# Performance work log

Hardware: AMD Instinct MI355X
Metric: run time of the kernel (lower is better)

## Reference

```python
import jax, jax.numpy as jnp
import numpy as np

G, K1, K2, N, NP, EPS = 16, 128, 32, 128, 512, 1e-5

def _bn(x, axes):
    m = jnp.mean(x, axes, keepdims=True)
    v = jnp.var(x, axes, keepdims=True)  # biased, as torch BN training mode
    return (x - m) * jax.lax.rsqrt(v + EPS)

def _fps(xyz, npoint):
    # farthest point sampling, deterministic start at index 0; xyz (B,P,3)
    B, P, _ = xyz.shape
    def step(carry, _):
        dists, far = carry
        c = jnp.take_along_axis(xyz, far[:, None, None], axis=1)   # (B,1,3)
        d = jnp.sum((xyz - c) ** 2, -1)                            # (B,P)
        dists = jnp.minimum(dists, d)
        return (dists, jnp.argmax(dists, -1)), far
    init = (jnp.full((B, P), 1e10, xyz.dtype), jnp.zeros((B,), jnp.int32))
    _, idx = jax.lax.scan(step, init, None, length=npoint)         # (npoint,B)
    return jnp.take_along_axis(xyz, idx.T[:, :, None], axis=1)     # (B,npoint,3)

def _pointnet(x, w1, b1, w2, b2, w3, b3):
    h = jax.nn.relu(_bn(x @ w1 + b1, (0, 1)))
    h = jax.nn.relu(_bn(h @ w2 + b2, (0, 1)))
    h = _bn(h @ w3 + b3, (0, 1))
    return jnp.max(h, axis=1)                                      # (B,1024)

def _mapping(feat, w1, b1, w2, b2, w3, b3, w4, b4):
    # all 16 branches stacked on leading axis g
    h = jax.nn.relu(_bn(jnp.einsum('bk,gkj->gbj', feat, w1) + b1[:, None, :], (1,)))
    h = jax.nn.relu(_bn(jnp.einsum('gbj,gjk->gbk', h, w2) + b2[:, None, :], (1,)))
    h = jax.nn.relu(_bn(jnp.einsum('gbj,gjk->gbk', h, w3) + b3[:, None, :], (1,)))
    return jax.nn.relu(_bn(jnp.einsum('gbj,gjk->gbk', h, w4) + b4[:, None, :], (1,)))

def _axform(feat, fw, fb, c1w, c1b, c2w, c2b, c3w, c3b, c4w, c4b):
    # feat (G,B,K1); 1x1 convs expressed as einsums in channels-last layout
    xb = (jnp.einsum('gbk,gkm->gbm', feat, fw) + fb[:, None, :]).reshape(G, -1, N, K2)
    h = jax.nn.relu(_bn(jnp.einsum('gbnk,gkc->gbnc', xb, c1w) + c1b[:, None, None, :], (1, 2)))
    h = jax.nn.relu(_bn(jnp.einsum('gbnc,gcd->gbnd', h, c2w) + c2b[:, None, None, :], (1, 2)))
    h = jnp.einsum('gbnd,gde->gbne', h, c3w) + c3b[:, None, None, :]  # (G,B,N,1024)
    w = jax.nn.softmax(h, axis=2)                                     # softmax over N
    y = jnp.einsum('gbne,gbnk->gbek', w, xb)                          # (G,B,1024,K2)
    return jnp.einsum('gbek,gkc->gbec', y, c4w) + c4b[:, None, None, :]  # (G,B,1024,3)

def _forward(x, pn, mp, gen, ref):
    x_partial = _fps(x, NP)                                           # (B,512,3)
    feat = _pointnet(x, *pn)                                          # (B,1024)
    mfeat = _mapping(feat, *mp)                                       # (G,B,K1)
    x1g = _axform(mfeat, *gen)                                        # (G,B,1024,3)
    B = x.shape[0]
    x_1 = jnp.transpose(x1g, (1, 0, 2, 3)).reshape(B, -1, 3)          # (B,16384,3)
    fps1 = jax.vmap(lambda p: _fps(p, NP))(x1g)                       # (G,B,512,3)
    x_base = jnp.concatenate([fps1, jnp.broadcast_to(x_partial, (G,) + x_partial.shape)], axis=2)
    x2g = x_base + _axform(mfeat, *ref)                               # (G,B,1024,3)
    x_2 = jnp.transpose(x2g, (1, 0, 2, 3)).reshape(B, -1, 3)
    return x_1, x_2

def setup_inputs() -> dict:
    keys = iter(jax.random.split(jax.random.key(0), 40))
    def rn(shape, s=0.02):
        return (s * jax.random.normal(next(keys), shape)).astype(jnp.float32)
    inp = {}
    inp['x'] = jax.random.normal(next(keys), (16, 2048, 3), jnp.float32)
    inp['pn_w1'] = rn((3, 64));      inp['pn_b1'] = rn((64,))
    inp['pn_w2'] = rn((64, 128));    inp['pn_b2'] = rn((128,))
    inp['pn_w3'] = rn((128, 1024));  inp['pn_b3'] = rn((1024,))
    inp['mp_w1'] = rn((G, 1024, 1024)); inp['mp_b1'] = rn((G, 1024))
    inp['mp_w2'] = rn((G, 1024, 1024)); inp['mp_b2'] = rn((G, 1024))
    inp['mp_w3'] = rn((G, 1024, 1024)); inp['mp_b3'] = rn((G, 1024))
    inp['mp_w4'] = rn((G, 1024, K1));   inp['mp_b4'] = rn((G, K1))
    for p in ('g', 'r'):
        inp[p + '_fw'] = rn((G, K1, N * K2)); inp[p + '_fb'] = rn((G, N * K2))
        inp[p + '_c1w'] = rn((G, K2, 64));    inp[p + '_c1b'] = rn((G, 64))
        inp[p + '_c2w'] = rn((G, 64, 128));   inp[p + '_c2b'] = rn((G, 128))
        inp[p + '_c3w'] = rn((G, 128, 1024)); inp[p + '_c3b'] = rn((G, 1024))
        inp[p + '_c4w'] = rn((G, K2, 3));     inp[p + '_c4b'] = rn((G, 3))
    return inp

def reference(x, pn_w1, pn_b1, pn_w2, pn_b2, pn_w3, pn_b3,
              mp_w1, mp_b1, mp_w2, mp_b2, mp_w3, mp_b3, mp_w4, mp_b4,
              g_fw, g_fb, g_c1w, g_c1b, g_c2w, g_c2b, g_c3w, g_c3b, g_c4w, g_c4b,
              r_fw, r_fb, r_c1w, r_c1b, r_c2w, r_c2b, r_c3w, r_c3b, r_c4w, r_c4b):
    pn = (pn_w1, pn_b1, pn_w2, pn_b2, pn_w3, pn_b3)
    mp = (mp_w1, mp_b1, mp_w2, mp_b2, mp_w3, mp_b3, mp_w4, mp_b4)
    gen = (g_fw, g_fb, g_c1w, g_c1b, g_c2w, g_c2b, g_c3w, g_c3b, g_c4w, g_c4b)
    ref = (r_fw, r_fb, r_c1w, r_c1b, r_c2w, r_c2b, r_c3w, r_c3b, r_c4w, r_c4b)
    return _forward(x, pn, mp, gen, ref)
```

## Files before the change

### kernel.cpp

```cpp
#include <hip/hip_runtime.h>
#include <math.h>

#define TID ((int)threadIdx.x)

namespace {
constexpr float EPSf = 1e-5f;

typedef __attribute__((ext_vector_type(8))) short short8;
typedef __attribute__((ext_vector_type(4))) float f32x4;

struct FpsArgs {
  const float* pts; float* out; float* dmin; int* far;
  int it0, it1, nc;
};

__device__ __forceinline__ unsigned fenc(float f){
  unsigned u = __float_as_uint(f);
  return (u & 0x80000000u) ? ~u : (u | 0x80000000u);
}
__device__ __forceinline__ float fdec(unsigned e){
  unsigned u = (e & 0x80000000u) ? (e & 0x7fffffffu) : ~e;
  return __uint_as_float(u);
}
__device__ __forceinline__ short bf16rne(float f){
  unsigned u = __float_as_uint(f);
  return (short)((u + 0x7fffu + ((u >> 16) & 1u)) >> 16);
}

template<int CTRL>
__device__ __forceinline__ void dpp_comb(float& bm, int& bp){
  int om_i = __builtin_amdgcn_update_dpp(__float_as_int(bm), __float_as_int(bm), CTRL, 0xf, 0xf, false);
  int op   = __builtin_amdgcn_update_dpp(bp, bp, CTRL, 0xf, 0xf, false);
  float om = __int_as_float(om_i);
  if (om > bm || (om == bm && op < bp)){ bm = om; bp = op; }
}

template<int LP, int NT>
__device__ void fps_body(const FpsArgs& a, int ci){
  const int NPTS = NT*LP;
  const float* pts = a.pts + (size_t)ci * NPTS * 3;
  float* out = a.out + (size_t)ci * 512 * 3;
  float* dst = a.dmin + (size_t)ci * NPTS;
  float px[LP], py[LP], pz[LP], dmin[LP];
#pragma unroll
  for (int j = 0; j < LP; j++){
    int p = TID + NT*j;
    px[j] = pts[p*3+0]; py[j] = pts[p*3+1]; pz[j] = pts[p*3+2];
  }
  int far;
  if (a.it0 == 0){
#pragma unroll
    for (int j = 0; j < LP; j++) dmin[j] = 1e10f;
    far = 0;
  } else {
#pragma unroll
    for (int j = 0; j < LP; j++) dmin[j] = dst[TID + NT*j];
    far = a.far[ci];
  }
  __shared__ unsigned long long red2[2][NT/64];
  for (int i = a.it0; i < a.it1; i++){
    float cx = pts[far*3+0], cy = pts[far*3+1], cz = pts[far*3+2];
    if (TID == 0){ out[i*3+0]=cx; out[i*3+1]=cy; out[i*3+2]=cz; }
    float bm = -1.f; int bp = 0;
#pragma unroll
    for (int j = 0; j < LP; j++){
      float dx = __fsub_rn(px[j], cx);
      float dy = __fsub_rn(py[j], cy);
      float dz = __fsub_rn(pz[j], cz);
      float d  = __fadd_rn(__fadd_rn(__fmul_rn(dx,dx), __fmul_rn(dy,dy)), __fmul_rn(dz,dz));
      float dm = fminf(dmin[j], d);
      dmin[j] = dm;
      if (dm > bm){ bm = dm; bp = TID + NT*j; }
    }
    dpp_comb<0x111>(bm,bp); dpp_comb<0x112>(bm,bp); dpp_comb<0x114>(bm,bp);
    dpp_comb<0x118>(bm,bp); dpp_comb<0x142>(bm,bp); dpp_comb<0x143>(bm,bp);
    unsigned long long key =
      ((unsigned long long)(unsigned)__builtin_amdgcn_readlane(__float_as_int(bm), 63) << 32)
      | (unsigned)~(unsigned)__builtin_amdgcn_readlane(bp, 63);
    if ((TID & 63) == 63) red2[i&1][TID>>6] = key;
    __syncthreads();
    unsigned long long kk = red2[i&1][0];
#pragma unroll
    for (int t = 1; t < NT/64; t++){
      unsigned long long o = red2[i&1][t];
      kk = kk > o ? kk : o;
    }
    far = (int)~(unsigned)kk;
  }
  if (a.it1 < 512){
#pragma unroll
    for (int j = 0; j < LP; j++) dst[TID + NT*j] = dmin[j];
    if (TID == 0) a.far[ci] = far;
  }
}

template<int LP>
__device__ void fps_wave(const FpsArgs& a, int ci){
  const int NPTS = 64*LP;
  int lane = TID & 63;
  const float* pts = a.pts + (size_t)ci * NPTS * 3;
  float* out = a.out + (size_t)ci * 512 * 3;
  float px[LP], py[LP], pz[LP], dmin[LP];
#pragma unroll
  for (int j = 0; j < LP; j++){
    int p = lane + 64*j;
    px[j] = pts[p*3+0]; py[j] = pts[p*3+1]; pz[j] = pts[p*3+2];
    dmin[j] = 1e10f;
  }
  int far = 0;
  for (int i = a.it0; i < a.it1; i++){
    float cx = pts[far*3+0], cy = pts[far*3+1], cz = pts[far*3+2];
    if (lane == 0){ out[i*3+0]=cx; out[i*3+1]=cy; out[i*3+2]=cz; }
    float bm = -1.f; int bp = 0;
#pragma unroll
    for (int j = 0; j < LP; j++){
      float dx = __fsub_rn(px[j], cx);
      float dy = __fsub_rn(py[j], cy);
      float dz = __fsub_rn(pz[j], cz);
      float d  = __fadd_rn(__fadd_rn(__fmul_rn(dx,dx), __fmul_rn(dy,dy)), __fmul_rn(dz,dz));
      float dm = fminf(dmin[j], d);
      dmin[j] = dm;
      if (dm > bm){ bm = dm; bp = lane + 64*j; }
    }
    dpp_comb<0x111>(bm,bp); dpp_comb<0x112>(bm,bp); dpp_comb<0x114>(bm,bp);
    dpp_comb<0x118>(bm,bp); dpp_comb<0x142>(bm,bp); dpp_comb<0x143>(bm,bp);
    far = __builtin_amdgcn_readlane(bp, 63);
  }
}

template<int C, int K, int FLP>
__global__ void __launch_bounds__(256) rowgemm_kernel(const float* __restrict__ in,
    const float* __restrict__ w, const float* __restrict__ bias, const float2* __restrict__ st2,
    float* __restrict__ out, int rows_per_g, FpsArgs fa)
{
  int bid = blockIdx.x;
  if constexpr (FLP > 0){
    if (bid < fa.nc){ fps_body<FLP,256>(fa, bid); return; }
    bid -= fa.nc;
  }
  constexpr int RPB = 256 / C;
  __shared__ float lin[RPB * K];
  size_t row0 = (size_t)bid * RPB;
  int g = (int)(row0 / rows_per_g);
  for (int i = TID; i < RPB*K; i += 256){
    float v = in[row0*(size_t)K + i];
    if (st2){ float2 s = st2[(size_t)g*K + (i % K)]; v = fmaxf((v - s.x)*s.y, 0.f); }
    lin[i] = v;
  }
  __syncthreads();
  int r = TID / C, c = TID % C;
  float acc = bias[(size_t)g*C + c];
  const float* wg = w + (size_t)g*K*C + c;
#pragma unroll
  for (int k = 0; k < K; k++) acc = fmaf(lin[r*K + k], wg[(size_t)k*C], acc);
  out[(row0 + r)*C + c] = acc;
}

template<int FLP>
__global__ void __launch_bounds__(256, 4) c2m_kernel(const float* __restrict__ in,
    const float2* __restrict__ st1, const short* __restrict__ wt,
    const float* __restrict__ bias, float* __restrict__ out, int rows_per_g, FpsArgs fa)
{
  int bid = blockIdx.x;
  if constexpr (FLP > 0){
    if (bid < fa.nc){ fps_body<FLP,256>(fa, bid); return; }
    bid -= fa.nc;
  }
  size_t row0 = (size_t)bid * 128;
  int g = (int)(row0 / rows_per_g);
  __shared__ short Bls[8192];
  __shared__ float2 sb[64];
  if (TID < 64) sb[TID] = st1[(size_t)g*64 + TID];
  {
    const short* wg = wt + (size_t)g*8192;
    for (int i = TID; i < 1024; i += 256){
      int c = i >> 3, kc = i & 7;
      short8 v = *(const short8*)&wg[c*64 + kc*8];
      *(short8*)&Bls[c*64 + ((kc ^ (c & 7)) << 3)] = v;
    }
  }
  __syncthreads();
  int lane = TID & 63, wid = TID >> 6, lr = lane & 15, lkg = lane >> 4;

  short8 afr[2][2];
  const float* src = in + row0*64;
#pragma unroll
  for (int kt = 0; kt < 2; kt++){
    int kb = kt*32 + lkg*8;
    float2 ss[8];
#pragma unroll
    for (int j = 0; j < 8; j++) ss[j] = sb[kb + j];
#pragma unroll
    for (int nt = 0; nt < 2; nt++){
      int row = wid*32 + nt*16 + lr;
      float4 a0 = *(const float4*)(src + row*64 + kb);
      float4 a1 = *(const float4*)(src + row*64 + kb + 4);
      const float vals[8] = {a0.x,a0.y,a0.z,a0.w,a1.x,a1.y,a1.z,a1.w};
      short8 ob;
#pragma unroll
      for (int j = 0; j < 8; j++)
        ob[j] = bf16rne(fmaxf((vals[j] - ss[j].x)*ss[j].y, 0.f));
      afr[kt][nt] = ob;
    }
  }

  f32x4 acc[2][8];
#pragma unroll
  for (int nt = 0; nt < 2; nt++)
#pragma unroll
    for (int et = 0; et < 8; et++) acc[nt][et] = (f32x4){0.f,0.f,0.f,0.f};
#pragma unroll
  for (int kt = 0; kt < 2; kt++){
#pragma unroll
    for (int et = 0; et < 8; et++){
      int e = et*16 + lr;
      short8 bfr = *(const short8*)&Bls[e*64 + (((kt*4 + lkg) ^ (e & 7)) << 3)];
      acc[0][et] = __builtin_amdgcn_mfma_f32_16x16x32_bf16(afr[kt][0], bfr, acc[0][et], 0, 0, 0);
      acc[1][et] = __builtin_amdgcn_mfma_f32_16x16x32_bf16(afr[kt][1], bfr, acc[1][et], 0, 0, 0);
    }
  }

#pragma unroll
  for (int et = 0; et < 8; et++){
    float bv = bias[(size_t)g*128 + et*16 + lr];
#pragma unroll
    for (int nt = 0; nt < 2; nt++)
#pragma unroll
      for (int r = 0; r < 4; r++){
        int row = wid*32 + nt*16 + lkg*4 + r;
        out[(row0 + row)*128 + et*16 + lr] = acc[nt][et][r] + bv;
      }
  }
}

template<int FLP>
__global__ void __launch_bounds__(256, 4) big1024m_kernel(const float* __restrict__ in,
    const float2* __restrict__ st2, const short* __restrict__ wtp,
    float* __restrict__ ps, float* __restrict__ pq, unsigned* __restrict__ maxenc, FpsArgs fa)
{
  int bid = blockIdx.x;
  if constexpr (FLP > 0){
    if (bid < fa.nc){ fps_body<FLP,256>(fa, bid); return; }
    bid -= fa.nc;
  }
  size_t row0 = (size_t)bid * 128;
  int b = (int)(row0 >> 11);
  __shared__ float2 sb[128];
  __shared__ float mS[512], mQ[512], mM[512];
  if (TID < 128) sb[TID] = st2[TID];
  __syncthreads();
  int lane = TID & 63, wid = TID >> 6, lr = lane & 15, lkg = lane >> 4;

  short8 afr[4][2];
  const float* src = in + row0*128;
#pragma unroll
  for (int kt = 0; kt < 4; kt++){
    int kb = kt*32 + lkg*8;
    float2 ss[8];
#pragma unroll
    for (int j = 0; j < 8; j++) ss[j] = sb[kb + j];
#pragma unroll
    for (int nt = 0; nt < 2; nt++){
      int row = wid*32 + nt*16 + lr;
      float4 a0 = *(const float4*)(src + row*128 + kb);
      float4 a1 = *(const float4*)(src + row*128 + kb + 4);
      const float vals[8] = {a0.x,a0.y,a0.z,a0.w,a1.x,a1.y,a1.z,a1.w};
      short8 ob;
#pragma unroll
      for (int j = 0; j < 8; j++)
        ob[j] = bf16rne(fmaxf((vals[j] - ss[j].x)*ss[j].y, 0.f));
      afr[kt][nt] = ob;
    }
  }

  for (int cs = 0; cs < 8; cs++){
    f32x4 acc[2][8];
#pragma unroll
    for (int nt = 0; nt < 2; nt++)
#pragma unroll
      for (int et = 0; et < 8; et++) acc[nt][et] = (f32x4){0.f,0.f,0.f,0.f};
    const short* wp = wtp + (size_t)(cs*128)*128;
#pragma unroll
    for (int kt = 0; kt < 4; kt++){
      int kb = kt*32 + lkg*8;
#pragma unroll
      for (int et = 0; et < 8; et++){
        short8 bfr = *(const short8*)&wp[(et*16 + lr)*128 + kb];
        acc[0][et] = __builtin_amdgcn_mfma_f32_16x16x32_bf16(afr[kt][0], bfr, acc[0][et], 0, 0, 0);
        acc[1][et] = __builtin_amdgcn_mfma_f32_16x16x32_bf16(afr[kt][1], bfr, acc[1][et], 0, 0, 0);
      }
    }
#pragma unroll
    for (int et = 0; et < 8; et++){
      float s = 0.f, q = 0.f, m = -1e38f;
#pragma unroll
      for (int nt = 0; nt < 2; nt++)
#pragma unroll
        for (int r = 0; r < 4; r++){
          float v = acc[nt][et][r];
          s += v; q = fmaf(v, v, q); m = fmaxf(m, v);
        }
      s += __shfl_xor(s, 16); s += __shfl_xor(s, 32);
      q += __shfl_xor(q, 16); q += __shfl_xor(q, 32);
      m = fmaxf(m, __shfl_xor(m, 16)); m = fmaxf(m, __shfl_xor(m, 32));
      if (lkg == 0){
        mS[wid*128 + et*16 + lr] = s;
        mQ[wid*128 + et*16 + lr] = q;
        mM[wid*128 + et*16 + lr] = m;
      }
    }
    __syncthreads();
    if (wid == 0){
#pragma unroll
      for (int t = 0; t < 2; t++){
        int c = t*64 + lane;
        float s4 = mS[c] + mS[128 + c] + mS[256 + c] + mS[384 + c];
        float q4 = mQ[c] + mQ[128 + c] + mQ[256 + c] + mQ[384 + c];
        float m4 = fmaxf(fmaxf(mM[c], mM[128 + c]), fmaxf(mM[256 + c], mM[384 + c]));
        ps[(size_t)bid*1024 + cs*128 + c] = s4;
        pq[(size_t)bid*1024 + cs*128 + c] = q4;
        atomicMax(&maxenc[(size_t)b*1024 + cs*128 + c], fenc(m4));
      }
    }
    __syncthreads();
  }
}

template<int FLP>
__global__ void __launch_bounds__(128) mapgemm2_kernel(const float* __restrict__ in, int in_gstride,
    const float* __restrict__ w, const float* __restrict__ bias, const float2* __restrict__ st2,
    float* __restrict__ out, int K, int J, int JB, int NS, FpsArgs fa)
{
  int bid = blockIdx.x;
  if constexpr (FLP > 0){
    if (bid < fa.nc){ fps_body<FLP,128>(fa, bid); return; }
    bid -= fa.nc;
  }
  int kc = bid / (JB*16);
  int g  = (bid / JB) % 16;
  int jb = bid % JB;
  int kchunk = K / NS, k0 = kc*kchunk;
  __shared__ float linT[128*16];
  const float* ing = in + (size_t)g * in_gstride;
  for (int i = TID; i < kchunk*16; i += 128){
    int b = i / kchunk, k = i - b*kchunk;
    float v = ing[(size_t)b*K + k0 + k];
    if (st2){ float2 s = st2[(size_t)g*K + k0 + k]; v = fmaxf((v - s.x)*s.y, 0.f); }
    linT[k*16 + b] = v;
  }
  __syncthreads();
  int bh = TID >> 6, jq = TID & 63;
  int j = jb*256 + jq*4;
  const float* wp = w + ((size_t)g*K + k0)*J + j;
  float4 a4[8];
#pragma unroll
  for (int bi = 0; bi < 8; bi++) a4[bi] = make_float4(0.f,0.f,0.f,0.f);
#pragma unroll 4
  for (int k = 0; k < kchunk; k++){
    float4 wv = *(const float4*)(wp + (size_t)k*J);
    float4 l0 = *(const float4*)&linT[k*16 + bh*8];
    float4 l1 = *(const float4*)&linT[k*16 + bh*8 + 4];
    const float lv[8] = {l0.x,l0.y,l0.z,l0.w,l1.x,l1.y,l1.z,l1.w};
#pragma unroll
    for (int bi = 0; bi < 8; bi++){
      a4[bi].x = fmaf(lv[bi], wv.x, a4[bi].x);
      a4[bi].y = fmaf(lv[bi], wv.y, a4[bi].y);
      a4[bi].z = fmaf(lv[bi], wv.z, a4[bi].z);
      a4[bi].w = fmaf(lv[bi], wv.w, a4[bi].w);
    }
  }
  if (NS == 1){
    float4 bv = *(const float4*)(bias + (size_t)g*J + j);
#pragma unroll
    for (int bi = 0; bi < 8; bi++){
      int b = bh*8 + bi;
      float4 o = make_float4(a4[bi].x+bv.x, a4[bi].y+bv.y, a4[bi].z+bv.z, a4[bi].w+bv.w);
      *(float4*)&out[((size_t)g*16 + b)*J + j] = o;
    }
  } else {
#pragma unroll
    for (int bi = 0; bi < 8; bi++)
      *(float4*)&out[(((size_t)kc*16 + g)*16 + bh*8 + bi)*J + j] = a4[bi];
  }
}

__global__ void __launch_bounds__(256) mapgemm_kernel(const float* __restrict__ in, int in_gstride,
    const float* __restrict__ w, const float* __restrict__ bias, const float2* __restrict__ st2,
    float* __restrict__ out, int K, int J, int JB, int NS)
{
  int bid = blockIdx.x;
  int kc = bid / (JB*16);
  int g  = (bid / JB) % 16;
  int jb = bid % JB;
  int j  = jb*256 + TID;
  bool jv = j < J;
  int jc = jv ? j : 0;
  int kchunk = K / NS;
  int k0 = kc * kchunk;
  __shared__ float lin[16 * 128];
  const float* ing = in + (size_t)g * in_gstride;
  float acc[16];
  float bv = (NS == 1 && jv) ? bias[(size_t)g*J + jc] : 0.f;
#pragma unroll
  for (int b = 0; b < 16; b++) acc[b] = bv;
  for (int kt = k0; kt < k0 + kchunk; kt += 128){
    __syncthreads();
    for (int i = TID; i < 2048; i += 256){
      int b = i >> 7, k = i & 127;
      float v = ing[(size_t)b*K + kt + k];
      if (st2){ float2 s = st2[(size_t)g*K + kt + k]; v = fmaxf((v - s.x)*s.y, 0.f); }
      lin[i] = v;
    }
    __syncthreads();
    const float* wg = w + ((size_t)g*K + kt)*J + jc;
    for (int k = 0; k < 128; k++){
      float wv = wg[(size_t)k*J];
#pragma unroll
      for (int b = 0; b < 16; b++) acc[b] = fmaf(lin[b*128 + k], wv, acc[b]);
    }
  }
  if (jv){
    if (NS == 1){
      for (int b = 0; b < 16; b++) out[((size_t)g*16 + b)*J + j] = acc[b];
    } else {
      for (int b = 0; b < 16; b++) out[(((size_t)kc*16 + g)*16 + b)*J + j] = acc[b];
    }
  }
}

__global__ void __launch_bounds__(256) redstats_kernel(const float* __restrict__ part,
    const float* __restrict__ bias, float* __restrict__ out, float2* __restrict__ st2,
    int J, int NS)
{
  int t = blockIdx.x*256 + TID;
  int g = t / J, j = t % J;
  float bv = bias[t];
  float s = 0.f, q = 0.f;
  for (int b = 0; b < 16; b++){
    float v = bv;
    for (int c = 0; c < NS; c++) v += part[(((size_t)c*16 + g)*16 + b)*J + j];
    out[((size_t)g*16 + b)*J + j] = v;
    s += v; q = fmaf(v, v, q);
  }
  float mean = s * (1.f/16.f);
  float var  = q * (1.f/16.f) - mean*mean;
  st2[t] = make_float2(mean, rsqrtf(fmaxf(var, 0.f) + EPSf));
}

template<int FLP>
__global__ void __launch_bounds__(256) statsacc_kernel(const float* __restrict__ in,
    float* __restrict__ part, int C, size_t chunk, FpsArgs fa)
{
  int bid = blockIdx.x;
  if constexpr (FLP > 0){
    if (bid < fa.nc){ fps_body<FLP,256>(fa, bid); return; }
    bid -= fa.nc;
  }
  size_t base = (size_t)bid * chunk;
  int c = TID % C;
  float s = 0.f, q = 0.f;
  for (size_t idx = base + TID; idx < base + chunk; idx += 256){
    float v = in[idx]; s += v; q = fmaf(v, v, q);
  }
  __shared__ float ls[256], lq[256];
  ls[TID] = s; lq[TID] = q; __syncthreads();
  if (TID < C){
    for (int t = TID + C; t < 256; t += C){ s += ls[t]; q += lq[t]; }
    part[((size_t)bid*C + c)*2]   = s;
    part[((size_t)bid*C + c)*2+1] = q;
  }
}

__global__ void statsfin_kernel(const float* __restrict__ part, float2* __restrict__ st2,
    int C, int G, float invR)
{
  int slot = blockIdx.x*256 + TID;
  if (slot >= G*C) return;
  int g = slot / C, c = slot % C;
  int bpg = 256 / G;
  float s = 0.f, q = 0.f;
  for (int b = 0; b < bpg; b++){
    size_t p = ((size_t)(g*bpg + b)*C + c)*2;
    s += part[p]; q += part[p+1];
  }
  float mean = s*invR;
  float var  = q*invR - mean*mean;
  st2[slot] = make_float2(mean, rsqrtf(fmaxf(var, 0.f) + EPSf));
}

__global__ void pnfin_kernel(const float* __restrict__ ps, const float* __restrict__ pq,
                             float2* __restrict__ st)
{
  int c = blockIdx.x*256 + TID;
  float s = 0.f, q = 0.f;
  for (int rb = 0; rb < 256; rb++){ s += ps[rb*1024 + c]; q += pq[rb*1024 + c]; }
  float mean = s * (1.f/32768.f);
  float var  = q * (1.f/32768.f) - mean*mean;
  st[c] = make_float2(mean, rsqrtf(fmaxf(var, 0.f) + EPSf));
}

__global__ void feat_kernel(const unsigned* __restrict__ me, const float2* __restrict__ st,
                            float* __restrict__ feat)
{
  int t = blockIdx.x*256 + TID;
  int c = t & 1023;
  float2 s = st[c];
  feat[t] = (fdec(me[t]) - s.x) * s.y;
}

__global__ void __launch_bounds__(256) wtr_kernel(const float* __restrict__ c3w,
                                                  short* __restrict__ wt)
{
  int g = blockIdx.x >> 4, kt = blockIdx.x & 15;
  __shared__ float lds[8*1024];
  const float* src = c3w + ((size_t)g*128 + kt*8)*1024;
  for (int i = TID; i < 8192; i += 256) lds[i] = src[i];
  __syncthreads();
  for (int e = TID; e < 1024; e += 256){
    short8 v;
#pragma unroll
    for (int j = 0; j < 8; j++) v[j] = bf16rne(lds[j*1024 + e]);
    *(short8*)&wt[((size_t)g*1024 + e)*128 + kt*8] = v;
  }
}

__global__ void __launch_bounds__(256) wtr2_kernel(const float* __restrict__ w,
                                                   short* __restrict__ wt)
{
  int g = blockIdx.x;
  __shared__ float lds[8192];
  const float* src = w + (size_t)g*8192;
  for (int i = TID; i < 8192; i += 256) lds[i] = src[i];
  __syncthreads();
  for (int i = TID; i < 1024; i += 256){
    int c = i >> 3, kc = i & 7;
    short8 v;
#pragma unroll
    for (int j = 0; j < 8; j++) v[j] = bf16rne(lds[(kc*8 + j)*128 + c]);
    *(short8*)&wt[(size_t)g*8192 + c*64 + kc*8] = v;
  }
}

template<int FLP>
__global__ void __launch_bounds__(256, 2) fused_kernel(const float* __restrict__ c2o,
    const float2* __restrict__ st2, const short* __restrict__ wt,
    const float* __restrict__ xb, const float* __restrict__ c4w, const float* __restrict__ c4b,
    float* __restrict__ out_pts, float* __restrict__ out_x1, FpsArgs fa)
{
  int bid = blockIdx.x;
  if constexpr (FLP > 0){
    if (bid < fa.nc){ fps_body<FLP,256>(fa, bid); return; }
    bid -= fa.nc;
  } else if constexpr (FLP < 0){
    if (bid < fa.nc){
      fps_wave<-FLP>(fa, bid*4 + (TID >> 6));
      return;
    }
    bid -= fa.nc;
  }
  int gb = bid >> 1, ebh = bid & 1;
  int g = gb >> 4, b = gb & 15;
  __shared__ short Pbf[16384];
  __shared__ short Bls[16384];
  __shared__ short xbT[4096];
  __shared__ float2 sb[128];
  __shared__ float mred[512];

  if (TID < 128) sb[TID] = st2[(size_t)g*128 + TID];
  {
    const float* xsrc = xb + (size_t)gb*4096;
    for (int idx = TID; idx < 1024; idx += 256){
      int n = idx >> 3, k4 = (idx & 7)*4;
      float4 v = *(const float4*)(xsrc + n*32 + k4);
      const float vv[4] = {v.x, v.y, v.z, v.w};
#pragma unroll
      for (int j = 0; j < 4; j++){
        int k = k4 + j;
        xbT[k*128 + (((n >> 3) ^ (k & 7)) << 3) + (n & 7)] = bf16rne(vv[j]);
      }
    }
  }
  const int eb0 = ebh*4;
  const short* wt_base = wt + (size_t)g*1024*128;
  {
    const short* wtg = wt_base + (size_t)(eb0*128)*128;
    for (int i = TID; i < 2048; i += 256){
      int e = i >> 4, kc = i & 15;
      short8 v = *(const short8*)&wtg[e*128 + kc*8];
      *(short8*)&Bls[e*128 + ((kc ^ (e & 7)) << 3)] = v;
    }
  }

  int lane = TID & 63, wid = TID >> 6;
  int lr = lane & 15, lkg = lane >> 4;

  __syncthreads();

  short8 afr[4][2];
  const float* src = c2o + (size_t)gb*16384;
#pragma unroll
  for (int kt = 0; kt < 4; kt++){
    int kb = kt*32 + lkg*8;
    float2 ss[8];
#pragma unroll
    for (int j = 0; j < 8; j++) ss[j] = sb[kb + j];
#pragma unroll
    for (int nt = 0; nt < 2; nt++){
      int row = wid*32 + nt*16 + lr;
      float4 a0 = *(const float4*)(src + row*128 + kb);
      float4 a1 = *(const float4*)(src + row*128 + kb + 4);
      const float vals[8] = {a0.x,a0.y,a0.z,a0.w,a1.x,a1.y,a1.z,a1.w};
      short8 ob;
#pragma unroll
      for (int j = 0; j < 8; j++)
        ob[j] = bf16rne(fmaxf((vals[j] - ss[j].x)*ss[j].y, 0.f));
      afr[kt][nt] = ob;
    }
  }

  float c4l[2][3];
  {
    const float* cw = c4w + g*96;
#pragma unroll
    for (int kt2 = 0; kt2 < 2; kt2++){
      int k = kt2*16 + lr;
      c4l[kt2][0] = cw[k*3+0]; c4l[kt2][1] = cw[k*3+1]; c4l[kt2][2] = cw[k*3+2];
    }
  }
  float cb0 = c4b[g*3+0], cb1 = c4b[g*3+1], cb2 = c4b[g*3+2];
  unsigned* Pu = (unsigned*)Pbf;

  for (int eb = eb0; eb < eb0 + 4; eb++){
    f32x4 acc[2][8];
#pragma unroll
    for (int nt = 0; nt < 2; nt++)
#pragma unroll
      for (int et = 0; et < 8; et++) acc[nt][et] = (f32x4){0.f,0.f,0.f,0.f};
#pragma unroll
    for (int kt = 0; kt < 4; kt++){
      int kcf = kt*4 + lkg;
#pragma unroll
      for (int et = 0; et < 8; et++){
        int e = et*16 + lr;
        short8 bfr = *(const short8*)&Bls[e*128 + ((kcf ^ (e & 7)) << 3)];
        acc[0][et] = __builtin_amdgcn_mfma_f32_16x16x32_bf16(afr[kt][0], bfr, acc[0][et], 0, 0, 0);
        acc[1][et] = __builtin_amdgcn_mfma_f32_16x16x32_bf16(afr[kt][1], bfr, acc[1][et], 0, 0, 0);
      }
    }

    short8 bpre[8];
    bool havepre = (eb + 1 < eb0 + 4);
    if (havepre){
      const short* wtg = wt_base + (size_t)((eb+1)*128)*128;
#pragma unroll
      for (int ii = 0; ii < 8; ii++){
        int i = TID + 256*ii;
        int e = i >> 4, kc = i & 15;
        bpre[ii] = *(const short8*)&wtg[e*128 + kc*8];
      }
    }

#pragma unroll
    for (int et = 0; et < 8; et++){
      float ss = 0.f;
#pragma unroll
      for (int nt = 0; nt < 2; nt++)
#pragma unroll
        for (int r = 0; r < 4; r++){
          float p = __expf(acc[nt][et][r]);
          acc[nt][et][r] = p;
          ss += p;
        }
      ss += __shfl_xor(ss, 16);
      ss += __shfl_xor(ss, 32);
      if (lkg == 0) mred[wid*128 + et*16 + lr] = ss;
      int e = et*16 + lr;
#pragma unroll
      for (int nt = 0; nt < 2; nt++){
        int nb = wid*32 + nt*16 + lkg*4;
        int base = e*128 + ((((nb >> 3)) ^ (e & 7)) << 3) + (nb & 7);
        unsigned lo = (unsigned)(unsigned short)bf16rne(acc[nt][et][0])
                    | ((unsigned)(unsigned short)bf16rne(acc[nt][et][1]) << 16);
        unsigned hi = (unsigned)(unsigned short)bf16rne(acc[nt][et][2])
                    | ((unsigned)(unsigned short)bf16rne(acc[nt][et][3]) << 16);
        Pu[base >> 1]       = lo;
        Pu[(base >> 1) + 1] = hi;
      }
    }
    __syncthreads();

    if (havepre){
#pragma unroll
      for (int ii = 0; ii < 8; ii++){
        int i = TID + 256*ii;
        int e = i >> 4, kc = i & 15;
        *(short8*)&Bls[e*128 + ((kc ^ (e & 7)) << 3)] = bpre[ii];
      }
    }

    f32x4 yy[2][2];
#pragma unroll
    for (int t2 = 0; t2 < 2; t2++){ yy[t2][0] = (f32x4){0.f,0.f,0.f,0.f}; yy[t2][1] = (f32x4){0.f,0.f,0.f,0.f}; }
#pragma unroll
    for (int nc = 0; nc < 4; nc++){
      short8 bfrs[2];
#pragma unroll
      for (int kt2 = 0; kt2 < 2; kt2++){
        int k = kt2*16 + lr;
        bfrs[kt2] = *(const short8*)&xbT[k*128 + (((nc*4 + lkg) ^ (k & 7)) << 3)];
      }
#pragma unroll
      for (int t2 = 0; t2 < 2; t2++){
        int e = (wid*2 + t2)*16 + lr;
        short8 afrp = *(const short8*)&Pbf[e*128 + (((nc*4 + lkg) ^ (e & 7)) << 3)];
        yy[t2][0] = __builtin_amdgcn_mfma_f32_16x16x32_bf16(afrp, bfrs[0], yy[t2][0], 0, 0, 0);
        yy[t2][1] = __builtin_amdgcn_mfma_f32_16x16x32_bf16(afrp, bfrs[1], yy[t2][1], 0, 0, 0);
      }
    }

#pragma unroll
    for (int t2 = 0; t2 < 2; t2++){
#pragma unroll
      for (int r = 0; r < 4; r++){
        float o0 = yy[t2][0][r]*c4l[0][0] + yy[t2][1][r]*c4l[1][0];
        float o1 = yy[t2][0][r]*c4l[0][1] + yy[t2][1][r]*c4l[1][1];
        float o2 = yy[t2][0][r]*c4l[0][2] + yy[t2][1][r]*c4l[1][2];
#pragma unroll
        for (int d = 1; d < 16; d <<= 1){
          o0 += __shfl_xor(o0, d);
          o1 += __shfl_xor(o1, d);
          o2 += __shfl_xor(o2, d);
        }
        if (lr == 0){
          int e = (wid*2 + t2)*16 + lkg*4 + r;
          float s = mred[e] + mred[128 + e] + mred[256 + e] + mred[384 + e];
          float rs = 1.f / s;
          o0 = fmaf(o0, rs, cb0);
          o1 = fmaf(o1, rs, cb1);
          o2 = fmaf(o2, rs, cb2);
          int eg = eb*128 + e;
          size_t po = ((size_t)gb*1024 + eg)*3;
          out_pts[po+0] = o0; out_pts[po+1] = o1; out_pts[po+2] = o2;
          if (out_x1){
            size_t xo = (((size_t)b*16 + g)*1024 + eg)*3;
            out_x1[xo+0] = o0; out_x1[xo+1] = o1; out_x1[xo+2] = o2;
          }
        }
      }
    }
    __syncthreads();
  }
}

__global__ void combine_kernel(const float* __restrict__ fps1, const float* __restrict__ xpart,
                               const float* __restrict__ d2, float* __restrict__ x2)
{
  size_t i = (size_t)blockIdx.x*256 + TID;
  if (i >= (size_t)16*16*1024*3) return;
  int c = (int)(i % 3);
  size_t t = i / 3;
  int e = (int)(t % 1024);
  size_t gb = t / 1024;
  int g = (int)(gb >> 4), b = (int)(gb & 15);
  float base;
  if (e < 512) base = fps1[(gb*512 + e)*3 + c];
  else         base = xpart[((size_t)b*512 + (e - 512))*3 + c];
  x2[(((size_t)b*16384) + (size_t)g*1024 + e)*3 + c] = base + d2[i];
}

}

extern "C" void kernel_launch(void* const* d_in, const int* in_sizes, int n_in,
                              void* d_out, int out_size, void* d_ws, size_t ws_size,
                              hipStream_t stream)
{
  (void)in_sizes; (void)n_in; (void)out_size; (void)ws_size;
  const float* x    = (const float*)d_in[0];
  const float* pnw1 = (const float*)d_in[1];
  const float* pnb1 = (const float*)d_in[2];
  const float* pnb2 = (const float*)d_in[4];
  const float* pnw3 = (const float*)d_in[5];
  const float* mpw[4] = {(const float*)d_in[7],(const float*)d_in[9],(const float*)d_in[11],(const float*)d_in[13]};
  const float* mpb[4] = {(const float*)d_in[8],(const float*)d_in[10],(const float*)d_in[12],(const float*)d_in[14]};

  float* ws = (float*)d_ws;
  size_t o = 0;
  auto alloc = [&](size_t n){ float* p = ws + o; o += n; return p; };
  float* x_partial = alloc(24576);
  float* feat      = alloc(16384);
  float* mfeat     = alloc(32768);
  float2* st_pn1   = (float2*)alloc(128);
  float2* st_pn2   = (float2*)alloc(256);
  float2* st_pn3   = (float2*)alloc(2048);
  float2* st_c1    = (float2*)alloc(2048);
  float2* st_c2    = (float2*)alloc(4096);
  float2* st_map0  = (float2*)alloc(32768);
  float2* st_map1  = (float2*)alloc(32768);
  float2* st_map2  = (float2*)alloc(32768);
  float2* st_map3  = (float2*)alloc(4096);
  float* sa_part   = alloc(65536);
  float* pn_ps     = alloc(262144);
  float* pn_pq     = alloc(262144);
  unsigned* maxenc = (unsigned*)alloc(16384);
  float* mapA      = alloc(262144);
  float* mapB      = alloc(262144);
  float* mpart     = alloc(4194304);
  float* xb        = alloc(1048576);
  float* c1o       = alloc(2097152);
  float* c2o       = alloc(4194304);
  float* x1g       = alloc(786432);
  float* d2buf     = alloc(786432);
  float* fps1b     = alloc(393216);
  float* fpsA_dmin = alloc(32768);
  int*   fpsA_far  = (int*)alloc(16);
  float* fpsB_dmin = alloc(262144);
  int*   fpsB_far  = (int*)alloc(256);
  short* wt_g      = (short*)alloc(1048576);
  short* wt_r      = (short*)alloc(1048576);
  short* wt_pn     = (short*)alloc(65536);
  short* wt_pn2    = (short*)alloc(4096);
  short* wt_c2g    = (short*)alloc(65536);
  short* wt_c2r    = (short*)alloc(65536);

  float* xout1 = (float*)d_out;
  float* xout2 = xout1 + 786432;

  hipMemsetAsync(maxenc, 0, 16384*sizeof(unsigned), stream);

  wtr_kernel<<<256, 256, 0, stream>>>((const float*)d_in[21], wt_g);
  wtr_kernel<<<256, 256, 0, stream>>>((const float*)d_in[31], wt_r);
  wtr_kernel<<<16, 256, 0, stream>>>(pnw3, wt_pn);
  wtr2_kernel<<<1, 256, 0, stream>>>((const float*)d_in[3],  wt_pn2);
  wtr2_kernel<<<16, 256, 0, stream>>>((const float*)d_in[19], wt_c2g);
  wtr2_kernel<<<16, 256, 0, stream>>>((const float*)d_in[29], wt_c2r);

  FpsArgs f0{};
  FpsArgs fa{x, x_partial, fpsA_dmin, fpsA_far, 0, 0, 16};

  fa.it0 = 0; fa.it1 = 64;
  rowgemm_kernel<64,3,8><<<8192+16, 256, 0, stream>>>(x, pnw1, pnb1, nullptr, c1o, 32768, fa);
  statsacc_kernel<0><<<256, 256, 0, stream>>>(c1o, sa_part, 64, 8192, f0);
  statsfin_kernel<<<1, 256, 0, stream>>>(sa_part, st_pn1, 64, 1, 1.f/32768.f);
  fa.it0 = 64; fa.it1 = 128;
  c2m_kernel<8><<<256+16, 256, 0, stream>>>(c1o, st_pn1, wt_pn2, pnb2, c2o, 32768, fa);
  statsacc_kernel<0><<<256, 256, 0, stream>>>(c2o, sa_part, 128, 16384, f0);
  statsfin_kernel<<<1, 256, 0, stream>>>(sa_part, st_pn2, 128, 1, 1.f/32768.f);
  fa.it0 = 128; fa.it1 = 224;
  big1024m_kernel<8><<<256+16, 256, 0, stream>>>(c2o, st_pn2, wt_pn, pn_ps, pn_pq, maxenc, fa);
  pnfin_kernel<<<4, 256, 0, stream>>>(pn_ps, pn_pq, st_pn3);
  feat_kernel<<<64, 256, 0, stream>>>(maxenc, st_pn3, feat);

  fa.it0 = 224; fa.it1 = 288;
  mapgemm2_kernel<16><<<1024+16, 128, 0, stream>>>(feat, 0,     mpw[0], nullptr, nullptr, mpart, 1024, 1024, 4, 16, fa);
  redstats_kernel<<<64, 256, 0, stream>>>(mpart, mpb[0], mapA, st_map0, 1024, 16);
  fa.it0 = 288; fa.it1 = 352;
  mapgemm2_kernel<16><<<1024+16, 128, 0, stream>>>(mapA, 16384, mpw[1], nullptr, st_map0, mpart, 1024, 1024, 4, 16, fa);
  redstats_kernel<<<64, 256, 0, stream>>>(mpart, mpb[1], mapB, st_map1, 1024, 16);
  fa.it0 = 352; fa.it1 = 416;
  mapgemm2_kernel<16><<<1024+16, 128, 0, stream>>>(mapB, 16384, mpw[2], nullptr, st_map1, mpart, 1024, 1024, 4, 16, fa);
  redstats_kernel<<<64, 256, 0, stream>>>(mpart, mpb[2], mapA, st_map2, 1024, 16);
  mapgemm_kernel<<<64, 256, 0, stream>>>(mapA, 16384, mpw[3], nullptr, st_map2, mpart, 1024, 128, 1, 4);
  redstats_kernel<<<8, 256, 0, stream>>>(mpart, mpb[3], mfeat, st_map3, 128, 4);

  for (int p = 0; p < 2; p++){
    const float* fw  = (const float*)d_in[15 + p*10 + 0];
    const float* fb  = (const float*)d_in[15 + p*10 + 1];
    const float* c1w = (const float*)d_in[15 + p*10 + 2];
    const float* c1b = (const float*)d_in[15 + p*10 + 3];
    const float* c2b = (const float*)d_in[15 + p*10 + 5];
    const float* c4w = (const float*)d_in[15 + p*10 + 8];
    const float* c4b = (const float*)d_in[15 + p*10 + 9];
    const short* wtc2 = (p == 0) ? wt_c2g : wt_c2r;

    if (p == 0){
      fa.it0 = 416; fa.it1 = 480;
      mapgemm2_kernel<16><<<256+16, 128, 0, stream>>>(mfeat, 2048, fw, fb, st_map3, xb, 128, 4096, 16, 1, fa);
      fa.it0 = 480; fa.it1 = 512;
      rowgemm_kernel<64,32,8><<<8192+16, 256, 0, stream>>>(xb, c1w, c1b, nullptr, c1o, 2048, fa);
      statsacc_kernel<0><<<256, 256, 0, stream>>>(c1o, sa_part, 64, 8192, f0);
      statsfin_kernel<<<4, 256, 0, stream>>>(sa_part, st_c1, 64, 16, 1.f/2048.f);
      c2m_kernel<0><<<256, 256, 0, stream>>>(c1o, st_c1, wtc2, c2b, c2o, 2048, f0);
      statsacc_kernel<0><<<256, 256, 0, stream>>>(c2o, sa_part, 128, 16384, f0);
      statsfin_kernel<<<8, 256, 0, stream>>>(sa_part, st_c2, 128, 16, 1.f/2048.f);
      fused_kernel<0><<<512, 256, 0, stream>>>(c2o, st_c2, wt_g, xb, c4w, c4b, x1g, xout1, f0);
    } else {
      mapgemm2_kernel<0><<<256, 128, 0, stream>>>(mfeat, 2048, fw, fb, st_map3, xb, 128, 4096, 16, 1, f0);
      rowgemm_kernel<64,32,0><<<8192, 256, 0, stream>>>(xb, c1w, c1b, nullptr, c1o, 2048, f0);
      statsacc_kernel<0><<<256, 256, 0, stream>>>(c1o, sa_part, 64, 8192, f0);
      statsfin_kernel<<<4, 256, 0, stream>>>(sa_part, st_c1, 64, 16, 1.f/2048.f);
      c2m_kernel<0><<<256, 256, 0, stream>>>(c1o, st_c1, wtc2, c2b, c2o, 2048, f0);
      statsacc_kernel<0><<<256, 256, 0, stream>>>(c2o, sa_part, 128, 16384, f0);
      statsfin_kernel<<<8, 256, 0, stream>>>(sa_part, st_c2, 128, 16, 1.f/2048.f);
      FpsArgs fb_{x1g, fps1b, fpsB_dmin, fpsB_far, 0, 512, 64};
      fused_kernel<-16><<<512+64, 256, 0, stream>>>(c2o, st_c2, wt_r, xb, c4w, c4b, d2buf, nullptr, fb_);
    }
  }

  combine_kernel<<<3072, 256, 0, stream>>>(fps1b, x_partial, d2buf, xout2);
}
```

Baseline: 1.713 ms.

## Spread second FPS across refine-stage kernels with resumable wave-level state

```diff
diff --git a/kernel.cpp b/kernel.cpp
--- a/kernel.cpp
+++ b/kernel.cpp
@@ -35,8 +35,23 @@
   if (om > bm || (om == bm && op < bp)){ bm = om; bp = op; }
 }
 
+template<int CTRL>
+__device__ __forceinline__ void dpp_comb5(float& bm, int& bp, float& bx, float& by, float& bz){
+  int om_i = __builtin_amdgcn_update_dpp(__float_as_int(bm), __float_as_int(bm), CTRL, 0xf, 0xf, false);
+  int op   = __builtin_amdgcn_update_dpp(bp, bp, CTRL, 0xf, 0xf, false);
+  int ox_i = __builtin_amdgcn_update_dpp(__float_as_int(bx), __float_as_int(bx), CTRL, 0xf, 0xf, false);
+  int oy_i = __builtin_amdgcn_update_dpp(__float_as_int(by), __float_as_int(by), CTRL, 0xf, 0xf, false);
+  int oz_i = __builtin_amdgcn_update_dpp(__float_as_int(bz), __float_as_int(bz), CTRL, 0xf, 0xf, false);
+  float om = __int_as_float(om_i);
+  if (om > bm || (om == bm && op < bp)){
+    bm = om; bp = op;
+    bx = __int_as_float(ox_i); by = __int_as_float(oy_i); bz = __int_as_float(oz_i);
+  }
+}
+
 template<int LP, int NT>
 __device__ void fps_body(const FpsArgs& a, int ci){
+  __builtin_amdgcn_s_setprio(1);
   const int NPTS = NT*LP;
   const float* pts = a.pts + (size_t)ci * NPTS * 3;
   float* out = a.out + (size_t)ci * 512 * 3;
@@ -92,26 +107,38 @@
     for (int j = 0; j < LP; j++) dst[TID + NT*j] = dmin[j];
     if (TID == 0) a.far[ci] = far;
   }
+  __builtin_amdgcn_s_setprio(0);
 }
 
 template<int LP>
 __device__ void fps_wave(const FpsArgs& a, int ci){
+  __builtin_amdgcn_s_setprio(1);
   const int NPTS = 64*LP;
   int lane = TID & 63;
   const float* pts = a.pts + (size_t)ci * NPTS * 3;
   float* out = a.out + (size_t)ci * 512 * 3;
+  float* dst = a.dmin + (size_t)ci * NPTS;
   float px[LP], py[LP], pz[LP], dmin[LP];
 #pragma unroll
   for (int j = 0; j < LP; j++){
     int p = lane + 64*j;
     px[j] = pts[p*3+0]; py[j] = pts[p*3+1]; pz[j] = pts[p*3+2];
-    dmin[j] = 1e10f;
-  }
-  int far = 0;
+  }
+  int far;
+  if (a.it0 == 0){
+#pragma unroll
+    for (int j = 0; j < LP; j++) dmin[j] = 1e10f;
+    far = 0;
+  } else {
+#pragma unroll
+    for (int j = 0; j < LP; j++) dmin[j] = dst[lane + 64*j];
+    far = a.far[ci];
+  }
+  float cx = pts[far*3+0], cy = pts[far*3+1], cz = pts[far*3+2];
   for (int i = a.it0; i < a.it1; i++){
-    float cx = pts[far*3+0], cy = pts[far*3+1], cz = pts[far*3+2];
     if (lane == 0){ out[i*3+0]=cx; out[i*3+1]=cy; out[i*3+2]=cz; }
     float bm = -1.f; int bp = 0;
+    float bx = 0.f, by = 0.f, bz = 0.f;
 #pragma unroll
     for (int j = 0; j < LP; j++){
       float dx = __fsub_rn(px[j], cx);
@@ -120,13 +147,35 @@
       float d  = __fadd_rn(__fadd_rn(__fmul_rn(dx,dx), __fmul_rn(dy,dy)), __fmul_rn(dz,dz));
       float dm = fminf(dmin[j], d);
       dmin[j] = dm;
-      if (dm > bm){ bm = dm; bp = lane + 64*j; }
-    }
-    dpp_comb<0x111>(bm,bp); dpp_comb<0x112>(bm,bp); dpp_comb<0x114>(bm,bp);
-    dpp_comb<0x118>(bm,bp); dpp_comb<0x142>(bm,bp); dpp_comb<0x143>(bm,bp);
+      if (dm > bm){ bm = dm; bp = lane + 64*j; bx = px[j]; by = py[j]; bz = pz[j]; }
+    }
+    dpp_comb5<0x111>(bm,bp,bx,by,bz); dpp_comb5<0x112>(bm,bp,bx,by,bz);
+    dpp_comb5<0x114>(bm,bp,bx,by,bz); dpp_comb5<0x118>(bm,bp,bx,by,bz);
+    dpp_comb5<0x142>(bm,bp,bx,by,bz); dpp_comb5<0x143>(bm,bp,bx,by,bz);
     far = __builtin_amdgcn_readlane(bp, 63);
-  }
-}
+    cx = __int_as_float(__builtin_amdgcn_readlane(__float_as_int(bx), 63));
+    cy = __int_as_float(__builtin_amdgcn_readlane(__float_as_int(by), 63));
+    cz = __int_as_float(__builtin_amdgcn_readlane(__float_as_int(bz), 63));
+  }
+  if (a.it1 < 512){
+#pragma unroll
+    for (int j = 0; j < LP; j++) dst[lane + 64*j] = dmin[j];
+    if (lane == 0) a.far[ci] = far;
+  }
+  __builtin_amdgcn_s_setprio(0);
+}
+
+#define FPS_SIDECAR(FLP, NT, fa, bid)                                        \
+  if constexpr (FLP > 0){                                                    \
+    if (bid < fa.nc){ fps_body<FLP, NT>(fa, bid); return; }                  \
+    bid -= fa.nc;                                                            \
+  } else if constexpr (FLP < 0){                                             \
+    if (bid < fa.nc){                                                        \
+      fps_wave<-FLP>(fa, bid*(NT >> 6) + (TID >> 6));                        \
+      return;                                                                \
+    }                                                                        \
+    bid -= fa.nc;                                                            \
+  }
 
 template<int C, int K, int FLP>
 __global__ void __launch_bounds__(256) rowgemm_kernel(const float* __restrict__ in,
@@ -134,10 +183,7 @@
     float* __restrict__ out, int rows_per_g, FpsArgs fa)
 {
   int bid = blockIdx.x;
-  if constexpr (FLP > 0){
-    if (bid < fa.nc){ fps_body<FLP,256>(fa, bid); return; }
-    bid -= fa.nc;
-  }
+  FPS_SIDECAR(FLP, 256, fa, bid)
   constexpr int RPB = 256 / C;
   __shared__ float lin[RPB * K];
   size_t row0 = (size_t)bid * RPB;
@@ -162,10 +208,7 @@
     const float* __restrict__ bias, float* __restrict__ out, int rows_per_g, FpsArgs fa)
 {
   int bid = blockIdx.x;
-  if constexpr (FLP > 0){
-    if (bid < fa.nc){ fps_body<FLP,256>(fa, bid); return; }
-    bid -= fa.nc;
-  }
+  FPS_SIDECAR(FLP, 256, fa, bid)
   size_t row0 = (size_t)bid * 128;
   int g = (int)(row0 / rows_per_g);
   __shared__ short Bls[8192];
@@ -239,10 +282,7 @@
     float* __restrict__ ps, float* __restrict__ pq, unsigned* __restrict__ maxenc, FpsArgs fa)
 {
   int bid = blockIdx.x;
-  if constexpr (FLP > 0){
-    if (bid < fa.nc){ fps_body<FLP,256>(fa, bid); return; }
-    bid -= fa.nc;
-  }
+  FPS_SIDECAR(FLP, 256, fa, bid)
   size_t row0 = (size_t)bid * 128;
   int b = (int)(row0 >> 11);
   __shared__ float2 sb[128];
@@ -332,10 +372,7 @@
     float* __restrict__ out, int K, int J, int JB, int NS, FpsArgs fa)
 {
   int bid = blockIdx.x;
-  if constexpr (FLP > 0){
-    if (bid < fa.nc){ fps_body<FLP,128>(fa, bid); return; }
-    bid -= fa.nc;
-  }
+  FPS_SIDECAR(FLP, 128, fa, bid)
   int kc = bid / (JB*16);
   int g  = (bid / JB) % 16;
   int jb = bid % JB;
@@ -452,10 +489,7 @@
     float* __restrict__ part, int C, size_t chunk, FpsArgs fa)
 {
   int bid = blockIdx.x;
-  if constexpr (FLP > 0){
-    if (bid < fa.nc){ fps_body<FLP,256>(fa, bid); return; }
-    bid -= fa.nc;
-  }
+  FPS_SIDECAR(FLP, 256, fa, bid)
   size_t base = (size_t)bid * chunk;
   int c = TID % C;
   float s = 0.f, q = 0.f;
@@ -548,16 +582,7 @@
     float* __restrict__ out_pts, float* __restrict__ out_x1, FpsArgs fa)
 {
   int bid = blockIdx.x;
-  if constexpr (FLP > 0){
-    if (bid < fa.nc){ fps_body<FLP,256>(fa, bid); return; }
-    bid -= fa.nc;
-  } else if constexpr (FLP < 0){
-    if (bid < fa.nc){
-      fps_wave<-FLP>(fa, bid*4 + (TID >> 6));
-      return;
-    }
-    bid -= fa.nc;
-  }
+  FPS_SIDECAR(FLP, 256, fa, bid)
   int gb = bid >> 1, ebh = bid & 1;
   int g = gb >> 4, b = gb & 15;
   __shared__ short Pbf[16384];
@@ -884,14 +909,20 @@
       statsfin_kernel<<<8, 256, 0, stream>>>(sa_part, st_c2, 128, 16, 1.f/2048.f);
       fused_kernel<0><<<512, 256, 0, stream>>>(c2o, st_c2, wt_g, xb, c4w, c4b, x1g, xout1, f0);
     } else {
-      mapgemm2_kernel<0><<<256, 128, 0, stream>>>(mfeat, 2048, fw, fb, st_map3, xb, 128, 4096, 16, 1, f0);
-      rowgemm_kernel<64,32,0><<<8192, 256, 0, stream>>>(xb, c1w, c1b, nullptr, c1o, 2048, f0);
-      statsacc_kernel<0><<<256, 256, 0, stream>>>(c1o, sa_part, 64, 8192, f0);
+      FpsArgs fb_{x1g, fps1b, fpsB_dmin, fpsB_far, 0, 0, 0};
+      fb_.it0 = 0;   fb_.it1 = 48;  fb_.nc = 128;
+      mapgemm2_kernel<-16><<<256+128, 128, 0, stream>>>(mfeat, 2048, fw, fb, st_map3, xb, 128, 4096, 16, 1, fb_);
+      fb_.it0 = 48;  fb_.it1 = 144; fb_.nc = 64;
+      rowgemm_kernel<64,32,-16><<<8192+64, 256, 0, stream>>>(xb, c1w, c1b, nullptr, c1o, 2048, fb_);
+      fb_.it0 = 144; fb_.it1 = 176;
+      statsacc_kernel<-16><<<256+64, 256, 0, stream>>>(c1o, sa_part, 64, 8192, fb_);
       statsfin_kernel<<<4, 256, 0, stream>>>(sa_part, st_c1, 64, 16, 1.f/2048.f);
-      c2m_kernel<0><<<256, 256, 0, stream>>>(c1o, st_c1, wtc2, c2b, c2o, 2048, f0);
-      statsacc_kernel<0><<<256, 256, 0, stream>>>(c2o, sa_part, 128, 16384, f0);
+      fb_.it0 = 176; fb_.it1 = 224;
+      c2m_kernel<-16><<<256+64, 256, 0, stream>>>(c1o, st_c1, wtc2, c2b, c2o, 2048, fb_);
+      fb_.it0 = 224; fb_.it1 = 256;
+      statsacc_kernel<-16><<<256+64, 256, 0, stream>>>(c2o, sa_part, 128, 16384, fb_);
       statsfin_kernel<<<8, 256, 0, stream>>>(sa_part, st_c2, 128, 16, 1.f/2048.f);
-      FpsArgs fb_{x1g, fps1b, fpsB_dmin, fpsB_far, 0, 512, 64};
+      fb_.it0 = 256; fb_.it1 = 512;
       fused_kernel<-16><<<512+64, 256, 0, stream>>>(c2o, st_c2, wt_r, xb, c4w, c4b, d2buf, nullptr, fb_);
     }
   }
```

New measurement: 1.667 ms. 1.03x faster.
